# Kernel optimization log

Hardware: AMD Instinct MI355X
Metric: run time of the kernel (lower is better)

## Reference

```python
import jax, jax.numpy as jnp
import numpy as np

N_EMBD = 256
BLOCK_SIZE = 128
N_HEAD = 8
HEAD_SIZE = 256
B = 256
T = 128


def setup_inputs() -> dict:
    key = jax.random.key(0)
    ks = jax.random.split(key, 9)
    s = 0.02
    return {
        "x": jax.random.normal(ks[0], (B, T, N_EMBD), dtype=jnp.float32),
        # torch Linear weight layout: [out_features, in_features], stacked over heads
        "Wq": jax.random.normal(ks[1], (N_HEAD, HEAD_SIZE, N_EMBD), dtype=jnp.float32) * s,
        "bq": jax.random.normal(ks[2], (N_HEAD, HEAD_SIZE), dtype=jnp.float32) * s,
        "Wk": jax.random.normal(ks[3], (N_HEAD, HEAD_SIZE, N_EMBD), dtype=jnp.float32) * s,
        "bk": jax.random.normal(ks[4], (N_HEAD, HEAD_SIZE), dtype=jnp.float32) * s,
        "Wv": jax.random.normal(ks[5], (N_HEAD, HEAD_SIZE, N_EMBD), dtype=jnp.float32) * s,
        "bv": jax.random.normal(ks[6], (N_HEAD, HEAD_SIZE), dtype=jnp.float32) * s,
        "Wp": jax.random.normal(ks[7], (N_EMBD, N_EMBD), dtype=jnp.float32) * s,
        "bp": jax.random.normal(ks[8], (N_EMBD,), dtype=jnp.float32) * s,
    }


def reference(x, Wq, bq, Wk, bk, Wv, bv, Wp, bp):
    Bb, Tt, C = x.shape
    scale = C ** (-0.5)  # NOTE: original scales by n_embd (input C), not head_size
    # per-head projections: [h, b, t, d]
    q = jnp.einsum("btc,hdc->hbtd", x, Wq) + bq[:, None, None, :]
    k = jnp.einsum("btc,hdc->hbtd", x, Wk) + bk[:, None, None, :]
    v = jnp.einsum("btc,hdc->hbtd", x, Wv) + bv[:, None, None, :]
    att = jnp.einsum("hbtd,hbsd->hbts", q, k) * scale  # [h,b,t,s]
    causal = jnp.tril(jnp.ones((Tt, Tt), dtype=bool))
    att = jnp.where(causal, att, -jnp.inf)
    att = jax.nn.softmax(att, axis=-1)
    out = jnp.einsum("hbts,hbsd->hbtd", att, v)
    # torch.cat along dim=0 (batch concat, as written in the source)
    out = out.reshape(out.shape[0] * Bb, Tt, out.shape[-1])  # [h*b, t, head_size]
    return out @ Wp.T + bp
```

## Files before the change

kernel.cpp:

```cpp
#include <hip/hip_runtime.h>
#include <hip/hip_bf16.h>
#include <stdint.h>


#define TT 128

typedef __attribute__((ext_vector_type(8))) short short8;
typedef __attribute__((ext_vector_type(4))) float f32x4;

#define WS_X    0u
#define WS_M    16777216u
#define WS_WM   17825792u
#define WS_WB   18874368u
#define WS_BB   18939904u
#define WS_CQ   18948096u

#define R_A    0
#define R_B    32768
#define R_UV   65536
#define R_RED  66560
#define LDS_SIZE 68608

#define LGKM0()  asm volatile("s_waitcnt lgkmcnt(0)" ::: "memory")
#define BAR()    do { asm volatile("" ::: "memory"); __builtin_amdgcn_s_barrier(); asm volatile("" ::: "memory"); } while (0)
#define PRIO1()  __builtin_amdgcn_s_setprio(1)
#define PRIO0()  __builtin_amdgcn_s_setprio(0)

__device__ __forceinline__ unsigned short f2bf(float x) {
    union { float f; unsigned u; } v; v.f = x;
    unsigned r = v.u + 0x7FFFu + ((v.u >> 16) & 1u);
    return (unsigned short)(r >> 16);
}
__device__ __forceinline__ unsigned pk2(float a, float b) {
    return (unsigned)f2bf(a) | ((unsigned)f2bf(b) << 16);
}

__global__ __launch_bounds__(256) void convert_pre(
    const float* __restrict__ x,
    const float* __restrict__ Wq, const float* __restrict__ bq,
    const float* __restrict__ Wk, const float* __restrict__ bk,
    const float* __restrict__ Wv, const float* __restrict__ bv,
    const float* __restrict__ Wp, const float* __restrict__ bp,
    char* __restrict__ ws)
{
    extern __shared__ char clds[];
    const int tid = threadIdx.x;
    const int bid = blockIdx.x;

    if (bid < 256) {
        const float* src = x + (size_t)bid * 32768;
        char* dst = ws + WS_X + (size_t)bid * 65536;
        for (int i = tid; i < 8192; i += 256) {
            float4 v = ((const float4*)src)[i];
            int row = i >> 6, c4 = i & 63;
            uint2 u; u.x = pk2(v.x, v.y); u.y = pk2(v.z, v.w);
            *(uint2*)(clds + row * 512 + ((c4 * 8) ^ ((row & 7) << 4))) = u;
        }
        __syncthreads();
        for (int i = tid; i < 4096; i += 256) {
            int l = i & 63, ks = (i >> 6) & 7, g = i >> 9;
            int r = g * 16 + (l & 15);
            int boff = ks * 64 + (l >> 4) * 16;
            uint4 q = *(const uint4*)(clds + r * 512 + (boff ^ ((r & 7) << 4)));
            ((uint4*)dst)[i] = q;
        }
        return;
    }
    if (bid < 384) {
        int id = bid - 256, h = id >> 4, st = id & 15;
        float* wkL = (float*)clds;
        for (int i = tid; i < 4096; i += 256) {
            int d = i >> 4, cc = i & 15;
            wkL[i] = Wk[(size_t)h * 65536 + d * 256 + st * 16 + cc];
        }
        __syncthreads();
        const int c = tid;
        float acc[16];
        #pragma unroll
        for (int j = 0; j < 16; ++j) acc[j] = 0.f;
        #pragma unroll 4
        for (int d = 0; d < 256; ++d) {
            float a = Wq[(size_t)h * 65536 + d * 256 + c];
            #pragma unroll
            for (int j = 0; j < 16; ++j) acc[j] += a * wkL[d * 16 + j];
        }
        char* base = ws + WS_M + (size_t)h * 131072;
        int ks = c >> 5, lgp = (c >> 3) & 3, jb = c & 7;
        #pragma unroll
        for (int j = 0; j < 16; ++j) {
            int cp = st * 16 + j;
            *(unsigned short*)(base + (((st * 8 + ks)) << 10)
                + ((cp & 15) + 16 * lgp) * 16 + jb * 2) = f2bf(acc[j] * 0.0625f);
        }
        return;
    }
    if (bid < 512) {
        int id = bid - 384, h = id >> 4, st = id & 15;
        float* wpL = (float*)clds;
        for (int i = tid; i < 4096; i += 256) {
            int e = i >> 8, d = i & 255;
            wpL[e * 257 + d] = Wp[(size_t)(st * 16 + e) * 256 + d];
        }
        __syncthreads();
        const int c = tid;
        float acc[16];
        #pragma unroll
        for (int j = 0; j < 16; ++j) acc[j] = 0.f;
        #pragma unroll 4
        for (int d = 0; d < 256; ++d) {
            float wv = Wv[(size_t)h * 65536 + d * 256 + c];
            #pragma unroll
            for (int j = 0; j < 16; ++j) acc[j] += wv * wpL[j * 257 + d];
        }
        char* base = ws + WS_WM + (size_t)h * 131072;
        int ks = c >> 5, lgp = (c >> 3) & 3, jb = c & 7;
        #pragma unroll
        for (int j = 0; j < 16; ++j) {
            *(unsigned short*)(base + (((st * 8 + ks)) << 10)
                + (j + 16 * lgp) * 16 + jb * 2) = f2bf(acc[j]);
        }
        return;
    }
    if (bid < 520) {
        const int h = bid - 512;
        {
            uint4 z = {0u,0u,0u,0u};
            for (int i = tid; i < 512; i += 256)
                ((uint4*)(ws + WS_WB + (size_t)h * 8192))[i] = z;
        }
        float* tK = (float*)clds;
        float* tQ = (float*)(clds + 16384);
        const int c = tid;
        float s1 = 0.f, s2 = 0.f;
        for (int d0 = 0; d0 < 256; d0 += 16) {
            __syncthreads();
            for (int i = tid; i < 1024; i += 256) {
                int row = i >> 6, c4 = i & 63;
                ((float4*)tK)[row * 64 + c4] =
                    ((const float4*)(Wk + (size_t)h * 65536 + (size_t)(d0 + row) * 256))[c4];
                ((float4*)tQ)[row * 64 + c4] =
                    ((const float4*)(Wq + (size_t)h * 65536 + (size_t)(d0 + row) * 256))[c4];
            }
            __syncthreads();
            #pragma unroll
            for (int dd = 0; dd < 16; ++dd) {
                s1 += tK[dd * 256 + c] * bq[h * 256 + d0 + dd];
                s2 += tQ[dd * 256 + c] * bk[h * 256 + d0 + dd];
            }
        }
        int ks = c >> 5, lgp = (c >> 3) & 3, jb = c & 7;
        char* base = ws + WS_WB + (size_t)h * 8192 + ks * 1024;
        *(unsigned short*)(base + (0 + 16 * lgp) * 16 + jb * 2) = f2bf(s2 * 0.0625f);
        *(unsigned short*)(base + (1 + 16 * lgp) * 16 + jb * 2) = f2bf(s1 * 0.0625f);
        float* red = (float*)(clds + 32768);
        red[tid] = bq[h * 256 + tid] * bk[h * 256 + tid];
        __syncthreads();
        if (tid == 0) {
            float cq = 0.f;
            for (int d = 0; d < 256; ++d) cq += red[d];
            *(float*)(ws + WS_CQ + h * 4) = cq * 0.0625f;
        }
        return;
    }
    {
        const int st = bid - 520;
        float* wpT = (float*)clds;
        float* bvL = (float*)(clds + 17408);
        for (int i = tid; i < 1024; i += 256) {
            int row = i >> 6, c4 = i & 63;
            float4 v = ((const float4*)(Wp + (size_t)(st * 16 + row) * 256))[c4];
            float* dstp = wpT + row * 257 + c4 * 4;
            dstp[0] = v.x; dstp[1] = v.y; dstp[2] = v.z; dstp[3] = v.w;
        }
        for (int i = tid; i < 512; i += 256)
            ((float4*)bvL)[i] = ((const float4*)bv)[i];
        __syncthreads();
        const int el = tid >> 4, dg = tid & 15;
        #pragma unroll
        for (int h = 0; h < 8; ++h) {
            float p = 0.f;
            #pragma unroll
            for (int dd = 0; dd < 16; ++dd) {
                int d = dg * 16 + dd;
                p += bvL[h * 256 + d] * wpT[el * 257 + d];
            }
            p += __shfl_xor(p, 1);
            p += __shfl_xor(p, 2);
            p += __shfl_xor(p, 4);
            p += __shfl_xor(p, 8);
            if (dg == 0)
                *(float*)(ws + WS_BB + (size_t)h * 1024 + (st * 16 + el) * 4)
                    = bp[st * 16 + el] + p;
        }
        return;
    }
}

__global__ __launch_bounds__(512, 1) void mha_fused(
    const char* __restrict__ ws, float* __restrict__ out)
{
    extern __shared__ char lds[];
    const int tid = threadIdx.x;
    const int w  = tid >> 6, l = tid & 63;
    const int lg = l >> 4, lr = l & 15;
    const int mq = w & 3, nh = w >> 2;
    const int bid = blockIdx.x;
    const int xcd = bid & 7, j = bid >> 3;
    const int h = j & 7;
    const int b = ((j >> 3) << 3) | xcd;
    const size_t orow = ((size_t)(h * 256 + b)) * TT;

    const char* Xf  = ws + WS_X  + (size_t)b * 65536;
    const char* Mh  = ws + WS_M  + (size_t)h * 131072;
    const char* WMh = ws + WS_WM + (size_t)h * 131072;
    const char* WBh = ws + WS_WB + (size_t)h * 8192;

    {
        f32x4 vacc[2] = {f32x4{0.f,0.f,0.f,0.f}, f32x4{0.f,0.f,0.f,0.f}};
        #pragma unroll
        for (int ks = 0; ks < 8; ++ks) {
            short8 wb  = *(const short8*)(WBh + (ks << 10) + l*16);
            short8 xa0 = *(const short8*)(Xf + (((mq*2 + 0)*8 + ks) << 10) + l*16);
            short8 xa1 = *(const short8*)(Xf + (((mq*2 + 1)*8 + ks) << 10) + l*16);
            vacc[0] = __builtin_amdgcn_mfma_f32_16x16x32_bf16(xa0, wb, vacc[0], 0, 0, 0);
            vacc[1] = __builtin_amdgcn_mfma_f32_16x16x32_bf16(xa1, wb, vacc[1], 0, 0, 0);
        }
        if (nh == 0 && lr < 2) {
            #pragma unroll
            for (int mt = 0; mt < 2; ++mt)
                #pragma unroll
                for (int r = 0; r < 4; ++r) {
                    int t = mq*32 + mt*16 + lg*4 + r;
                    *(float*)(lds + R_UV + lr*512 + t*4) = vacc[mt][r];
                }
        }
    }

    #pragma unroll
    for (int p2 = 0; p2 < 2; ++p2) {
        const int ga = p2*8 + nh*4;
        f32x4 acc[2][4];
        #pragma unroll
        for (int i = 0; i < 2; ++i)
            #pragma unroll
            for (int jj = 0; jj < 4; ++jj) acc[i][jj] = f32x4{0.f,0.f,0.f,0.f};
        #pragma unroll
        for (int ks = 0; ks < 8; ++ks) {
            short8 xa[2];
            #pragma unroll
            for (int mt = 0; mt < 2; ++mt)
                xa[mt] = *(const short8*)(Xf + (((mq*2 + mt)*8 + ks) << 10) + l*16);
            short8 nb[4];
            #pragma unroll
            for (int nt = 0; nt < 4; ++nt)
                nb[nt] = *(const short8*)(Mh + (((ga+nt)*8 + ks) << 10) + l*16);
            PRIO1();
            #pragma unroll
            for (int mt = 0; mt < 2; ++mt)
                #pragma unroll
                for (int nt = 0; nt < 4; ++nt)
                    acc[mt][nt] = __builtin_amdgcn_mfma_f32_16x16x32_bf16(xa[mt], nb[nt], acc[mt][nt], 0, 0, 0);
            PRIO0();
        }
        #pragma unroll
        for (int mt = 0; mt < 2; ++mt)
            #pragma unroll
            for (int nt = 0; nt < 4; ++nt)
                #pragma unroll
                for (int r = 0; r < 4; ++r) {
                    int t = mq*32 + mt*16 + lg*4 + r;
                    int cp = (ga+nt)*16 + lr;
                    *(unsigned short*)(lds + R_A + t*512 + ((cp*2) ^ ((t&7)<<4)))
                        = f2bf(acc[mt][nt][r]);
                }
    }
    LGKM0(); BAR();

    f32x4 sacc[2][4];
    #pragma unroll
    for (int i = 0; i < 2; ++i)
        #pragma unroll
        for (int jj = 0; jj < 4; ++jj) sacc[i][jj] = f32x4{0.f,0.f,0.f,0.f};
    #pragma unroll
    for (int ks2 = 0; ks2 < 8; ++ks2) {
        short8 ta[2];
        #pragma unroll
        for (int mt = 0; mt < 2; ++mt) {
            int t2 = mq*32 + mt*16 + lr;
            ta[mt] = *(const short8*)(lds + R_A + t2*512 + ((ks2*64 + lg*16) ^ ((t2&7)<<4)));
        }
        short8 sb[4];
        #pragma unroll
        for (int nt = 0; nt < 4; ++nt)
            sb[nt] = *(const short8*)(Xf + (((nh*4+nt)*8 + ks2) << 10) + l*16);
        PRIO1();
        #pragma unroll
        for (int mt = 0; mt < 2; ++mt)
            #pragma unroll
            for (int nt = 0; nt < 4; ++nt)
                sacc[mt][nt] = __builtin_amdgcn_mfma_f32_16x16x32_bf16(ta[mt], sb[nt], sacc[mt][nt], 0, 0, 0);
        PRIO0();
    }

    {
        const float cq = *(const float*)(ws + WS_CQ + h*4);
        float uu[4];
        #pragma unroll
        for (int nt = 0; nt < 4; ++nt)
            uu[nt] = *(const float*)(lds + R_UV + 512 + (nh*64 + nt*16 + lr)*4);
        float* redM = (float*)(lds + R_RED);
        float* redS = redM + 256;
        float rmax[2][4];
        #pragma unroll
        for (int mt = 0; mt < 2; ++mt)
            #pragma unroll
            for (int r = 0; r < 4; ++r) {
                int t = mq*32 + mt*16 + lg*4 + r;
                float vt = *(const float*)(lds + R_UV + t*4) + cq;
                float m = -1e30f;
                #pragma unroll
                for (int nt = 0; nt < 4; ++nt) {
                    int s = nh*64 + nt*16 + lr;
                    float sv = sacc[mt][nt][r] + vt + uu[nt];
                    if (s > t) sv = -1e30f;
                    sacc[mt][nt][r] = sv;
                    m = fmaxf(m, sv);
                }
                m = fmaxf(m, __shfl_xor(m, 1));
                m = fmaxf(m, __shfl_xor(m, 2));
                m = fmaxf(m, __shfl_xor(m, 4));
                m = fmaxf(m, __shfl_xor(m, 8));
                rmax[mt][r] = m;
            }
        if (lr == 0) {
            #pragma unroll
            for (int mt = 0; mt < 2; ++mt)
                #pragma unroll
                for (int r = 0; r < 4; ++r)
                    redM[nh*128 + mq*32 + mt*16 + lg*4 + r] = rmax[mt][r];
        }
        LGKM0(); BAR();
        float rsum[2][4];
        #pragma unroll
        for (int mt = 0; mt < 2; ++mt)
            #pragma unroll
            for (int r = 0; r < 4; ++r) {
                int t = mq*32 + mt*16 + lg*4 + r;
                float m = fmaxf(redM[t], redM[128 + t]);
                float ssum = 0.f;
                #pragma unroll
                for (int nt = 0; nt < 4; ++nt) {
                    float p = __expf(sacc[mt][nt][r] - m);
                    sacc[mt][nt][r] = p;
                    ssum += p;
                }
                ssum += __shfl_xor(ssum, 1);
                ssum += __shfl_xor(ssum, 2);
                ssum += __shfl_xor(ssum, 4);
                ssum += __shfl_xor(ssum, 8);
                rsum[mt][r] = ssum;
            }
        if (lr == 0) {
            #pragma unroll
            for (int mt = 0; mt < 2; ++mt)
                #pragma unroll
                for (int r = 0; r < 4; ++r)
                    redS[nh*128 + mq*32 + mt*16 + lg*4 + r] = rsum[mt][r];
        }
        LGKM0(); BAR();
        #pragma unroll
        for (int mt = 0; mt < 2; ++mt)
            #pragma unroll
            for (int r = 0; r < 4; ++r) {
                int t = mq*32 + mt*16 + lg*4 + r;
                float inv = 1.0f / (redS[t] + redS[128 + t]);
                #pragma unroll
                for (int nt = 0; nt < 4; ++nt) {
                    int s = nh*64 + nt*16 + lr;
                    *(unsigned short*)(lds + R_A + t*256 + ((s*2) ^ ((t&7)<<4)))
                        = f2bf(sacc[mt][nt][r] * inv);
                }
            }
    }
    LGKM0(); BAR();

    short8 pa[2][4];
    #pragma unroll
    for (int mt = 0; mt < 2; ++mt) {
        int t2 = mq*32 + mt*16 + lr;
        #pragma unroll
        for (int ks = 0; ks < 4; ++ks)
            pa[mt][ks] = *(const short8*)(lds + R_A + t2*256 + ((ks*64 + lg*16) ^ ((t2&7)<<4)));
    }

    const float* bbp = (const float*)(ws + WS_BB + h*1024);
    #pragma unroll
    for (int eh = 0; eh < 2; ++eh) {
        {
            f32x4 acc[2][4];
            #pragma unroll
            for (int i = 0; i < 2; ++i)
                #pragma unroll
                for (int jj = 0; jj < 4; ++jj) acc[i][jj] = f32x4{0.f,0.f,0.f,0.f};
            #pragma unroll
            for (int ks = 0; ks < 8; ++ks) {
                short8 wa[2];
                #pragma unroll
                for (int me = 0; me < 2; ++me)
                    wa[me] = *(const short8*)(WMh + (((eh*8 + mq*2+me)*8 + ks) << 10) + l*16);
                short8 sb[4];
                #pragma unroll
                for (int nt = 0; nt < 4; ++nt)
                    sb[nt] = *(const short8*)(Xf + (((nh*4 + nt)*8 + ks) << 10) + l*16);
                PRIO1();
                #pragma unroll
                for (int me = 0; me < 2; ++me)
                    #pragma unroll
                    for (int nt = 0; nt < 4; ++nt)
                        acc[me][nt] = __builtin_amdgcn_mfma_f32_16x16x32_bf16(wa[me], sb[nt], acc[me][nt], 0, 0, 0);
                PRIO0();
            }
            #pragma unroll
            for (int me = 0; me < 2; ++me)
                #pragma unroll
                for (int nt = 0; nt < 4; ++nt)
                    #pragma unroll
                    for (int r = 0; r < 4; ++r) {
                        int el = (mq*2+me)*16 + lg*4 + r;
                        int s  = (nh*4 + nt)*16 + lr;
                        *(unsigned short*)(lds + R_B + el*256 + ((s*2) ^ ((el&7)<<4)))
                            = f2bf(acc[me][nt][r]);
                    }
        }
        LGKM0(); BAR();
        #pragma unroll
        for (int ec = 0; ec < 2; ++ec) {
            f32x4 acc[2][2];
            #pragma unroll
            for (int i = 0; i < 2; ++i)
                #pragma unroll
                for (int jj = 0; jj < 2; ++jj) acc[i][jj] = f32x4{0.f,0.f,0.f,0.f};
            #pragma unroll
            for (int ks = 0; ks < 4; ++ks) {
                short8 hb[2];
                #pragma unroll
                for (int nt = 0; nt < 2; ++nt) {
                    int erl = (nh*4 + ec*2 + nt)*16 + lr;
                    hb[nt] = *(const short8*)(lds + R_B + erl*256 + ((ks*64 + lg*16) ^ ((erl&7)<<4)));
                }
                PRIO1();
                #pragma unroll
                for (int mt = 0; mt < 2; ++mt)
                    #pragma unroll
                    for (int nt = 0; nt < 2; ++nt)
                        acc[mt][nt] = __builtin_amdgcn_mfma_f32_16x16x32_bf16(pa[mt][ks], hb[nt], acc[mt][nt], 0, 0, 0);
                PRIO0();
            }
            #pragma unroll
            for (int nt = 0; nt < 2; ++nt) {
                int e = eh*128 + (nh*4 + ec*2 + nt)*16 + lr;
                float bbv = bbp[e];
                #pragma unroll
                for (int mt = 0; mt < 2; ++mt)
                    #pragma unroll
                    for (int r = 0; r < 4; ++r) {
                        int t = mq*32 + mt*16 + lg*4 + r;
                        out[(orow + t) * 256 + e] = acc[mt][nt][r] + bbv;
                    }
            }
        }
        if (eh == 0) { LGKM0(); BAR(); }
    }
}

extern "C" void kernel_launch(void* const* d_in, const int* in_sizes, int n_in,
                              void* d_out, int out_size, void* d_ws, size_t ws_size,
                              hipStream_t stream) {
    (void)in_sizes; (void)n_in; (void)out_size; (void)ws_size;
    const float* x  = (const float*)d_in[0];
    const float* Wq = (const float*)d_in[1];
    const float* bq = (const float*)d_in[2];
    const float* Wk = (const float*)d_in[3];
    const float* bk = (const float*)d_in[4];
    const float* Wv = (const float*)d_in[5];
    const float* bv = (const float*)d_in[6];
    const float* Wp = (const float*)d_in[7];
    const float* bp = (const float*)d_in[8];
    char* ws = (char*)d_ws;

    hipFuncSetAttribute((const void*)convert_pre,
                        hipFuncAttributeMaxDynamicSharedMemorySize, 65536);
    convert_pre<<<dim3(536), dim3(256), 65536, stream>>>(
        x, Wq, bq, Wk, bk, Wv, bv, Wp, bp, ws);

    hipFuncSetAttribute((const void*)mha_fused,
                        hipFuncAttributeMaxDynamicSharedMemorySize, LDS_SIZE);
    mha_fused<<<dim3(2048), dim3(512), LDS_SIZE, stream>>>(ws, (float*)d_out);
}
```

Baseline: 279.1 us.

## Stage per-batch X tile in LDS via global_load_lds and retile projection GEMMs

After: 267.2 us. 1.04x faster.

```diff
diff --git a/kernel.cpp b/kernel.cpp
--- a/kernel.cpp
+++ b/kernel.cpp
@@ -15,16 +15,22 @@
 #define WS_BB   18939904u
 #define WS_CQ   18948096u
 
-#define R_A    0
-#define R_B    32768
-#define R_UV   65536
-#define R_RED  66560
-#define LDS_SIZE 68608
-
+#define LX     0
+#define LT     65536
+#define LP     65536
+#define LH     98304
+#define R_UV   131072
+#define R_RED  132096
+#define LDS_SIZE 134144
+
+#define VMCNT0() asm volatile("s_waitcnt vmcnt(0)" ::: "memory")
 #define LGKM0()  asm volatile("s_waitcnt lgkmcnt(0)" ::: "memory")
 #define BAR()    do { asm volatile("" ::: "memory"); __builtin_amdgcn_s_barrier(); asm volatile("" ::: "memory"); } while (0)
 #define PRIO1()  __builtin_amdgcn_s_setprio(1)
 #define PRIO0()  __builtin_amdgcn_s_setprio(0)
+
+typedef __attribute__((address_space(3))) uint32_t lds_u32;
+typedef __attribute__((address_space(1))) const uint32_t glb_u32;
 
 __device__ __forceinline__ unsigned short f2bf(float x) {
     union { float f; unsigned u; } v; v.f = x;
@@ -216,12 +222,21 @@
     const char* WBh = ws + WS_WB + (size_t)h * 8192;
 
     {
+        const char* src = Xf + tid * 16;
+        #pragma unroll
+        for (int p = 0; p < 8; ++p)
+            __builtin_amdgcn_global_load_lds((glb_u32*)(src + p * 8192),
+                (lds_u32*)(lds + LX + tid * 16 + p * 8192), 16, 0, 0);
+    }
+    VMCNT0(); BAR();
+
+    {
         f32x4 vacc[2] = {f32x4{0.f,0.f,0.f,0.f}, f32x4{0.f,0.f,0.f,0.f}};
         #pragma unroll
         for (int ks = 0; ks < 8; ++ks) {
             short8 wb  = *(const short8*)(WBh + (ks << 10) + l*16);
-            short8 xa0 = *(const short8*)(Xf + (((mq*2 + 0)*8 + ks) << 10) + l*16);
-            short8 xa1 = *(const short8*)(Xf + (((mq*2 + 1)*8 + ks) << 10) + l*16);
+            short8 xa0 = *(const short8*)(lds + LX + (((mq*2 + 0)*8 + ks) << 10) + l*16);
+            short8 xa1 = *(const short8*)(lds + LX + (((mq*2 + 1)*8 + ks) << 10) + l*16);
             vacc[0] = __builtin_amdgcn_mfma_f32_16x16x32_bf16(xa0, wb, vacc[0], 0, 0, 0);
             vacc[1] = __builtin_amdgcn_mfma_f32_16x16x32_bf16(xa1, wb, vacc[1], 0, 0, 0);
         }
@@ -237,42 +252,31 @@
     }
 
     #pragma unroll
-    for (int p2 = 0; p2 < 2; ++p2) {
-        const int ga = p2*8 + nh*4;
-        f32x4 acc[2][4];
-        #pragma unroll
-        for (int i = 0; i < 2; ++i)
-            #pragma unroll
-            for (int jj = 0; jj < 4; ++jj) acc[i][jj] = f32x4{0.f,0.f,0.f,0.f};
+    for (int pass = 0; pass < 2; ++pass) {
+        const int ga = w*2 + pass;
+        f32x4 acc[8];
+        #pragma unroll
+        for (int i = 0; i < 8; ++i) acc[i] = f32x4{0.f,0.f,0.f,0.f};
         #pragma unroll
         for (int ks = 0; ks < 8; ++ks) {
-            short8 xa[2];
-            #pragma unroll
-            for (int mt = 0; mt < 2; ++mt)
-                xa[mt] = *(const short8*)(Xf + (((mq*2 + mt)*8 + ks) << 10) + l*16);
-            short8 nb[4];
-            #pragma unroll
-            for (int nt = 0; nt < 4; ++nt)
-                nb[nt] = *(const short8*)(Mh + (((ga+nt)*8 + ks) << 10) + l*16);
+            short8 nb = *(const short8*)(Mh + (((ga*8 + ks)) << 10) + l*16);
             PRIO1();
             #pragma unroll
-            for (int mt = 0; mt < 2; ++mt)
-                #pragma unroll
-                for (int nt = 0; nt < 4; ++nt)
-                    acc[mt][nt] = __builtin_amdgcn_mfma_f32_16x16x32_bf16(xa[mt], nb[nt], acc[mt][nt], 0, 0, 0);
+            for (int mt = 0; mt < 8; ++mt) {
+                short8 xa = *(const short8*)(lds + LX + (((mt*8 + ks)) << 10) + l*16);
+                acc[mt] = __builtin_amdgcn_mfma_f32_16x16x32_bf16(xa, nb, acc[mt], 0, 0, 0);
+            }
             PRIO0();
         }
         #pragma unroll
-        for (int mt = 0; mt < 2; ++mt)
-            #pragma unroll
-            for (int nt = 0; nt < 4; ++nt)
-                #pragma unroll
-                for (int r = 0; r < 4; ++r) {
-                    int t = mq*32 + mt*16 + lg*4 + r;
-                    int cp = (ga+nt)*16 + lr;
-                    *(unsigned short*)(lds + R_A + t*512 + ((cp*2) ^ ((t&7)<<4)))
-                        = f2bf(acc[mt][nt][r]);
-                }
+        for (int mt = 0; mt < 8; ++mt)
+            #pragma unroll
+            for (int r = 0; r < 4; ++r) {
+                int t = mt*16 + lg*4 + r;
+                int c = ga*16 + lr;
+                *(unsigned short*)(lds + LT + t*512 + ((c*2) ^ ((t&7)<<4)))
+                    = f2bf(acc[mt][r]);
+            }
     }
     LGKM0(); BAR();
 
@@ -287,12 +291,12 @@
         #pragma unroll
         for (int mt = 0; mt < 2; ++mt) {
             int t2 = mq*32 + mt*16 + lr;
-            ta[mt] = *(const short8*)(lds + R_A + t2*512 + ((ks2*64 + lg*16) ^ ((t2&7)<<4)));
+            ta[mt] = *(const short8*)(lds + LT + t2*512 + ((ks2*64 + lg*16) ^ ((t2&7)<<4)));
         }
         short8 sb[4];
         #pragma unroll
         for (int nt = 0; nt < 4; ++nt)
-            sb[nt] = *(const short8*)(Xf + (((nh*4+nt)*8 + ks2) << 10) + l*16);
+            sb[nt] = *(const short8*)(lds + LX + (((nh*4+nt)*8 + ks2) << 10) + l*16);
         PRIO1();
         #pragma unroll
         for (int mt = 0; mt < 2; ++mt)
@@ -377,7 +381,7 @@
                 #pragma unroll
                 for (int nt = 0; nt < 4; ++nt) {
                     int s = nh*64 + nt*16 + lr;
-                    *(unsigned short*)(lds + R_A + t*256 + ((s*2) ^ ((t&7)<<4)))
+                    *(unsigned short*)(lds + LP + t*256 + ((s*2) ^ ((t&7)<<4)))
                         = f2bf(sacc[mt][nt][r] * inv);
                 }
             }
@@ -390,47 +394,36 @@
         int t2 = mq*32 + mt*16 + lr;
         #pragma unroll
         for (int ks = 0; ks < 4; ++ks)
-            pa[mt][ks] = *(const short8*)(lds + R_A + t2*256 + ((ks*64 + lg*16) ^ ((t2&7)<<4)));
+            pa[mt][ks] = *(const short8*)(lds + LP + t2*256 + ((ks*64 + lg*16) ^ ((t2&7)<<4)));
     }
 
     const float* bbp = (const float*)(ws + WS_BB + h*1024);
     #pragma unroll
     for (int eh = 0; eh < 2; ++eh) {
         {
-            f32x4 acc[2][4];
-            #pragma unroll
-            for (int i = 0; i < 2; ++i)
-                #pragma unroll
-                for (int jj = 0; jj < 4; ++jj) acc[i][jj] = f32x4{0.f,0.f,0.f,0.f};
+            f32x4 acc[8];
+            #pragma unroll
+            for (int i = 0; i < 8; ++i) acc[i] = f32x4{0.f,0.f,0.f,0.f};
             #pragma unroll
             for (int ks = 0; ks < 8; ++ks) {
-                short8 wa[2];
-                #pragma unroll
-                for (int me = 0; me < 2; ++me)
-                    wa[me] = *(const short8*)(WMh + (((eh*8 + mq*2+me)*8 + ks) << 10) + l*16);
-                short8 sb[4];
-                #pragma unroll
-                for (int nt = 0; nt < 4; ++nt)
-                    sb[nt] = *(const short8*)(Xf + (((nh*4 + nt)*8 + ks) << 10) + l*16);
+                short8 wa = *(const short8*)(WMh + ((((eh*8 + w)*8 + ks)) << 10) + l*16);
                 PRIO1();
                 #pragma unroll
-                for (int me = 0; me < 2; ++me)
-                    #pragma unroll
-                    for (int nt = 0; nt < 4; ++nt)
-                        acc[me][nt] = __builtin_amdgcn_mfma_f32_16x16x32_bf16(wa[me], sb[nt], acc[me][nt], 0, 0, 0);
+                for (int nt = 0; nt < 8; ++nt) {
+                    short8 sb = *(const short8*)(lds + LX + (((nt*8 + ks)) << 10) + l*16);
+                    acc[nt] = __builtin_amdgcn_mfma_f32_16x16x32_bf16(wa, sb, acc[nt], 0, 0, 0);
+                }
                 PRIO0();
             }
             #pragma unroll
-            for (int me = 0; me < 2; ++me)
-                #pragma unroll
-                for (int nt = 0; nt < 4; ++nt)
-                    #pragma unroll
-                    for (int r = 0; r < 4; ++r) {
-                        int el = (mq*2+me)*16 + lg*4 + r;
-                        int s  = (nh*4 + nt)*16 + lr;
-                        *(unsigned short*)(lds + R_B + el*256 + ((s*2) ^ ((el&7)<<4)))
-                            = f2bf(acc[me][nt][r]);
-                    }
+            for (int nt = 0; nt < 8; ++nt)
+                #pragma unroll
+                for (int r = 0; r < 4; ++r) {
+                    int el = w*16 + lg*4 + r;
+                    int s  = nt*16 + lr;
+                    *(unsigned short*)(lds + LH + el*256 + ((s*2) ^ ((el&7)<<4)))
+                        = f2bf(acc[nt][r]);
+                }
         }
         LGKM0(); BAR();
         #pragma unroll
@@ -446,7 +439,7 @@
                 #pragma unroll
                 for (int nt = 0; nt < 2; ++nt) {
                     int erl = (nh*4 + ec*2 + nt)*16 + lr;
-                    hb[nt] = *(const short8*)(lds + R_B + erl*256 + ((ks*64 + lg*16) ^ ((erl&7)<<4)));
+                    hb[nt] = *(const short8*)(lds + LH + erl*256 + ((ks*64 + lg*16) ^ ((erl&7)<<4)));
                 }
                 PRIO1();
                 #pragma unroll
```
